# Kernel tuning notes

Measured on AMD Instinct MI355X. Metric: run time of the kernel, lower is better.

## Reference

```python
import jax, jax.numpy as jnp
import numpy as np

BLOCK_SIZE = 50  # from module globals


def setup_inputs() -> dict:
    key = jax.random.key(0)
    ks = jax.random.split(key, 5)
    B, T, C, H = 8, 1024, 512, 64
    return {
        "x": jax.random.normal(ks[0], (B, T, C), dtype=jnp.float32),
        "Wq": jax.random.normal(ks[1], (C, H), dtype=jnp.float32) * (C ** -0.5),
        "Wk": jax.random.normal(ks[2], (C, H), dtype=jnp.float32) * (C ** -0.5),
        "Wv": jax.random.normal(ks[3], (C, H), dtype=jnp.float32) * (C ** -0.5),
        "rel_pos_emb": jax.random.normal(ks[4], (2 * BLOCK_SIZE - 1, H), dtype=jnp.float32),
    }


def reference(x, Wq, Wk, Wv, rel_pos_emb):
    # x: [B, T, C]; dropout is identity in eval mode.
    B, T, C = x.shape
    q = x @ Wq  # [B, T, H]
    k = x @ Wk
    v = x @ Wv
    H = q.shape[-1]

    # relative position indices, clamped to window, shifted to [0, 2*block-2]
    t = jnp.arange(T)
    rel = jnp.clip(t[None, :] - t[:, None], -(BLOCK_SIZE - 1), BLOCK_SIZE - 1) + (BLOCK_SIZE - 1)
    E = rel_pos_emb[rel]  # [T, T, H]

    scale = H ** -0.5
    # content scores (scaled) + relative-position bias (unscaled, per source)
    wei = jnp.einsum("btd,bsd->bts", q, k) * scale + jnp.einsum("btd,tsd->bts", q, E)

    causal = t[None, :] <= t[:, None]  # [T, T] lower-triangular True
    wei = jnp.where(causal[None, :, :], wei, -jnp.inf)
    wei = jax.nn.softmax(wei, axis=-1)
    return jnp.einsum("bts,bsd->btd", wei, v)
```

## Files before the change

kernel.cpp:

```cpp
#include <hip/hip_runtime.h>
#include <hip/hip_bf16.h>

typedef __bf16 bf16x8 __attribute__((ext_vector_type(8)));
typedef float  f32x4  __attribute__((ext_vector_type(4)));

#define MFMA16(a, b, c) __builtin_amdgcn_mfma_f32_16x16x32_bf16(a, b, c, 0, 0, 0)

static __device__ __forceinline__ f32x4 zero4() {
    f32x4 z = {0.f, 0.f, 0.f, 0.f}; return z;
}

#define FIXED_MAX 37.0f

__global__ __launch_bounds__(512) void prep_kernel(
        const float* __restrict__ x,
        const float* __restrict__ Wq, const float* __restrict__ Wk,
        const float* __restrict__ Wv, const float* __restrict__ rpe,
        __bf16* __restrict__ WT_hi, __bf16* __restrict__ WT_lo,
        __bf16* __restrict__ xh, __bf16* __restrict__ xl) {
    int blk = blockIdx.x, tid = threadIdx.x;
    if (blk < 256) {
        int n = blk, k = tid;
        float v;
        if (n < 192) {
            const float* src; int nc;
            if (n < 64)       { src = Wq; nc = n; }
            else if (n < 128) { src = Wk; nc = n - 64; }
            else              { src = Wv; nc = n - 128; }
            v = src[k * 64 + nc];
        } else {
            int nc = n - 192;
            const f32x4* rp = (const f32x4*)(rpe + nc * 64);
            const f32x4* w0 = (const f32x4*)(Wq + k * 64);
            float a0 = 0.f;
#pragma unroll
            for (int i = 0; i < 16; i++) {
                f32x4 r = rp[i], x0 = w0[i];
                a0 += x0.x * r.x + x0.y * r.y + x0.z * r.z + x0.w * r.w;
            }
            v = a0;
        }
        __bf16 h = (__bf16)v;
        WT_hi[n * 512 + k] = h;
        WT_lo[n * 512 + k] = (__bf16)(v - (float)h);
    } else {
        size_t base = (size_t)(blk - 256) * 4096;
        const f32x4* xp = (const f32x4*)(x + base);
        f32x4 a0 = xp[2 * tid], a1 = xp[2 * tid + 1];
        bf16x8 h8, l8;
#pragma unroll
        for (int e = 0; e < 4; e++) {
            float v = a0[e]; __bf16 h = (__bf16)v;
            h8[e] = h; l8[e] = (__bf16)(v - (float)h);
            v = a1[e]; h = (__bf16)v;
            h8[4 + e] = h; l8[4 + e] = (__bf16)(v - (float)h);
        }
        *(bf16x8*)(xh + base + (size_t)tid * 8) = h8;
        *(bf16x8*)(xl + base + (size_t)tid * 8) = l8;
    }
}

__global__ __launch_bounds__(512) void proj_kernel(
        const __bf16* __restrict__ xh, const __bf16* __restrict__ xl,
        const __bf16* __restrict__ WT_hi, const __bf16* __restrict__ WT_lo,
        __bf16* __restrict__ qb, __bf16* __restrict__ kb,
        __bf16* __restrict__ vtb, float* __restrict__ qEg) {
    __shared__ f32x4 accx[4][64][4];

    int tid = threadIdx.x;
    int lane = tid & 63, w = tid >> 6;
    int c = w & 3, kh = w >> 2;
    int l15 = lane & 15, kg = lane >> 4;
    int rowA = blockIdx.x * 16 + l15;
    const __bf16* xhrow = xh + (size_t)rowA * 512;
    const __bf16* xlrow = xl + (size_t)rowA * 512;

    f32x4 acc[4];
#pragma unroll
    for (int i = 0; i < 4; i++) acc[i] = zero4();

#pragma unroll
    for (int ks8 = 0; ks8 < 8; ks8++) {
        int k0 = (kh * 8 + ks8) * 32 + kg * 8;
        bf16x8 xhf = *(const bf16x8*)(xhrow + k0);
        bf16x8 xlf = *(const bf16x8*)(xlrow + k0);
#pragma unroll
        for (int i = 0; i < 4; i++) {
            int nt = c + 4 * i;
            const __bf16* bp = WT_hi + (size_t)(nt * 16 + l15) * 512 + k0;
            bf16x8 bh = *(const bf16x8*)bp;
            acc[i] = MFMA16(xhf, bh, acc[i]);
            if (i == 0 || i == 3) {
                bf16x8 bl = *(const bf16x8*)(WT_lo + (size_t)(nt * 16 + l15) * 512 + k0);
                acc[i] = MFMA16(xhf, bl, acc[i]);
                acc[i] = MFMA16(xlf, bh, acc[i]);
            }
        }
    }

    if (kh == 1) {
#pragma unroll
        for (int i = 0; i < 4; i++) accx[c][lane][i] = acc[i];
    }
    __syncthreads();
    if (kh == 0) {
#pragma unroll
        for (int i = 0; i < 4; i++) {
            f32x4 o = accx[c][lane][i];
            acc[i].x += o.x; acc[i].y += o.y; acc[i].z += o.z; acc[i].w += o.w;
        }
        int rowO = blockIdx.x * 16 + kg * 4;
#pragma unroll
        for (int i = 0; i < 4; i++) {
            int cc = (c * 16 + l15) & 63;
#pragma unroll
            for (int r = 0; r < 4; r++) {
                float v = acc[i][r];
                int row = rowO + r;
                if (i == 0) {
                    qb[row * 64 + cc] = (__bf16)v;
                } else if (i == 1) {
                    kb[row * 64 + cc] = (__bf16)v;
                } else if (i == 2) {
                    int bb = row >> 10, s = row & 1023;
                    vtb[((size_t)(bb * 64 + cc) << 10) + s] = (__bf16)v;
                } else {
                    qEg[row * 64 + cc] = v;
                }
            }
        }
    }
}

__global__ __launch_bounds__(512) void attn_kernel(
        const __bf16* __restrict__ qb, const __bf16* __restrict__ kb,
        const __bf16* __restrict__ vtb, const float* __restrict__ qEg,
        float* __restrict__ out) {
    __shared__ float  Opart[8][16][68];
    __shared__ float  lpart[8][16];
    __shared__ float  qEs[16][52];
    __shared__ __bf16 Plds[8][16][72];

    int tid = threadIdx.x;
    int lane = tid & 63, w = tid >> 6;
    int l15 = lane & 15, kg = lane >> 4;
    int b = blockIdx.x & 7, p = blockIdx.x >> 3;
    int bT = b << 10;
    const __bf16* vbase = vtb + ((size_t)b << 16);

    int qts0 = 63 - p, qts1 = p;
#pragma unroll 1
    for (int qi = 0; qi < 2; qi++) {
        int qt = (qi == 0) ? qts0 : qts1;

        for (int idx = tid; idx < 16 * 50; idx += 512) {
            int r = idx / 50, j = idx - r * 50;
            qEs[r][j] = qEg[(bT + qt * 16 + r) * 64 + j];
        }
        __syncthreads();

        int qrow = bT + qt * 16 + l15;
        bf16x8 qf0 = *(const bf16x8*)(qb + (size_t)qrow * 64 + kg * 8);
        bf16x8 qf1 = *(const bf16x8*)(qb + (size_t)qrow * 64 + 32 + kg * 8);

        f32x4 O[4]; float prs[4];
#pragma unroll
        for (int i = 0; i < 4; i++) { O[i] = zero4(); prs[i] = 0.f; }

        int nt = (qt >> 2) + 1;
        for (int it = w; it < nt; it += 8) {
            int sb = it * 64;
            f32x4 s[4];
#pragma unroll
            for (int ct = 0; ct < 4; ct++) {
                const __bf16* kp = kb + (size_t)(bT + sb + ct * 16 + l15) * 64 + kg * 8;
                bf16x8 kf0 = *(const bf16x8*)kp;
                bf16x8 kf1 = *(const bf16x8*)(kp + 32);
                f32x4 z = zero4();
                z = MFMA16(qf0, kf0, z);
                s[ct] = MFMA16(qf1, kf1, z);
            }

            float pm[4][4];
#pragma unroll
            for (int r = 0; r < 4; r++) {
                int tg = qt * 16 + kg * 4 + r;
#pragma unroll
                for (int ct = 0; ct < 4; ct++) {
                    int sg = sb + ct * 16 + l15;
                    int d = sg - tg;
                    int j = d < -49 ? -49 : d;
                    j = (j > 0 ? 0 : j) + 49;
                    float lg = s[ct][r] * 0.125f + qEs[kg * 4 + r][j] - FIXED_MAX;
                    float pv = (d > 0) ? 0.f : __expf(lg);
                    pm[r][ct] = pv;
                    prs[r] += pv;
                }
            }

#pragma unroll
            for (int r = 0; r < 4; r++)
#pragma unroll
                for (int ct = 0; ct < 4; ct++)
                    Plds[w][kg * 4 + r][ct * 16 + l15] = (__bf16)pm[r][ct];

#pragma unroll
            for (int ks = 0; ks < 2; ks++) {
                bf16x8 af = *(const bf16x8*)&Plds[w][l15][ks * 32 + kg * 8];
#pragma unroll
                for (int dt = 0; dt < 4; dt++) {
                    bf16x8 vf = *(const bf16x8*)(vbase +
                        ((size_t)(dt * 16 + l15) << 10) + sb + ks * 32 + kg * 8);
                    O[dt] = MFMA16(af, vf, O[dt]);
                }
            }
        }

#pragma unroll
        for (int r = 0; r < 4; r++) {
            float v = prs[r];
            v += __shfl_xor(v, 1);
            v += __shfl_xor(v, 2);
            v += __shfl_xor(v, 4);
            v += __shfl_xor(v, 8);
            if (l15 == 0) lpart[w][kg * 4 + r] = v;
#pragma unroll
            for (int dt = 0; dt < 4; dt++)
                Opart[w][kg * 4 + r][dt * 16 + l15] = O[dt][r];
        }
        __syncthreads();

#pragma unroll
        for (int e = 0; e < 2; e++) {
            int elem = tid + e * 512;
            int row = elem >> 6, d = elem & 63;
            float os = 0.f, ls = 0.f;
#pragma unroll
            for (int wv = 0; wv < 8; wv++) {
                os += Opart[wv][row][d];
                ls += lpart[wv][row];
            }
            out[(size_t)(bT + qt * 16 + row) * 64 + d] = os / ls;
        }
        __syncthreads();
    }
}

extern "C" void kernel_launch(void* const* d_in, const int* in_sizes, int n_in,
                              void* d_out, int out_size, void* d_ws, size_t ws_size,
                              hipStream_t stream) {
    const float* x   = (const float*)d_in[0];
    const float* Wq  = (const float*)d_in[1];
    const float* Wk  = (const float*)d_in[2];
    const float* Wv  = (const float*)d_in[3];
    const float* rpe = (const float*)d_in[4];

    char* ws = (char*)d_ws;
    __bf16* WT_hi = (__bf16*)(ws);
    __bf16* WT_lo = (__bf16*)(ws + (256 << 10));
    __bf16* qbuf  = (__bf16*)(ws + (512 << 10));
    __bf16* kbuf  = (__bf16*)(ws + (1536 << 10));
    __bf16* vtb   = (__bf16*)(ws + (2560 << 10));
    float*  qEg   = (float*)(ws + (3584 << 10));
    __bf16* xhb   = (__bf16*)(ws + (6 << 20));
    __bf16* xlb   = (__bf16*)(ws + (14 << 20));
    float*  outp  = (float*)d_out;

    hipLaunchKernelGGL(prep_kernel, dim3(1280), dim3(512), 0, stream,
                       x, Wq, Wk, Wv, rpe, WT_hi, WT_lo, xhb, xlb);
    hipLaunchKernelGGL(proj_kernel, dim3(512), dim3(512), 0, stream,
                       xhb, xlb, WT_hi, WT_lo, qbuf, kbuf, vtb, qEg);
    hipLaunchKernelGGL(attn_kernel, dim3(256), dim3(512), 0, stream,
                       qbuf, kbuf, vtb, qEg, outp);
}
```

Baseline: 122.9 us.

## Fuse prep, projection and attention into one cooperative kernel with grid syncs

Replaces the three launches with one cooperative kernel of 256 blocks that uses grid.sync between phases. The x hi/lo bf16 split now goes into swizzled shared memory instead of a global scratch buffer, and each block projects 32 rows without the split-K LDS reduction. This removes launch gaps and the global round trip of the split x buffers. In exchange it adds grid-wide barrier cost, fewer blocks and waves in the projection phase, and 64KB of LDS per block that may limit occupancy.

```diff
diff --git a/kernel.cpp b/kernel.cpp
--- a/kernel.cpp
+++ b/kernel.cpp
@@ -1,5 +1,8 @@
 #include <hip/hip_runtime.h>
 #include <hip/hip_bf16.h>
+#include <hip/hip_cooperative_groups.h>
+
+namespace cg = cooperative_groups;
 
 typedef __bf16 bf16x8 __attribute__((ext_vector_type(8)));
 typedef float  f32x4  __attribute__((ext_vector_type(4)));
@@ -12,14 +15,32 @@
 
 #define FIXED_MAX 37.0f
 
-__global__ __launch_bounds__(512) void prep_kernel(
+union SMem {
+    struct { char xh[32768]; char xl[32768]; } p12;
+    struct {
+        float  Opart[8][16][68];
+        float  lpart[8][16];
+        float  qEs[16][52];
+        __bf16 Plds[8][16][72];
+    } p3;
+};
+
+__global__ __launch_bounds__(512) void fused_kernel(
         const float* __restrict__ x,
         const float* __restrict__ Wq, const float* __restrict__ Wk,
         const float* __restrict__ Wv, const float* __restrict__ rpe,
         __bf16* __restrict__ WT_hi, __bf16* __restrict__ WT_lo,
-        __bf16* __restrict__ xh, __bf16* __restrict__ xl) {
+        __bf16* __restrict__ qb, __bf16* __restrict__ kb,
+        __bf16* __restrict__ vtb, float* __restrict__ qEg,
+        float* __restrict__ out) {
+    __shared__ SMem sm;
+    cg::grid_group grid = cg::this_grid();
+
     int blk = blockIdx.x, tid = threadIdx.x;
-    if (blk < 256) {
+    int lane = tid & 63, w = tid >> 6;
+    int l15 = lane & 15, kg = lane >> 4;
+
+    {
         int n = blk, k = tid;
         float v;
         if (n < 192) {
@@ -43,76 +64,65 @@
         __bf16 h = (__bf16)v;
         WT_hi[n * 512 + k] = h;
         WT_lo[n * 512 + k] = (__bf16)(v - (float)h);
-    } else {
-        size_t base = (size_t)(blk - 256) * 4096;
-        const f32x4* xp = (const f32x4*)(x + base);
-        f32x4 a0 = xp[2 * tid], a1 = xp[2 * tid + 1];
-        bf16x8 h8, l8;
-#pragma unroll
-        for (int e = 0; e < 4; e++) {
-            float v = a0[e]; __bf16 h = (__bf16)v;
-            h8[e] = h; l8[e] = (__bf16)(v - (float)h);
-            v = a1[e]; h = (__bf16)v;
-            h8[4 + e] = h; l8[4 + e] = (__bf16)(v - (float)h);
-        }
-        *(bf16x8*)(xh + base + (size_t)tid * 8) = h8;
-        *(bf16x8*)(xl + base + (size_t)tid * 8) = l8;
-    }
-}
-
-__global__ __launch_bounds__(512) void proj_kernel(
-        const __bf16* __restrict__ xh, const __bf16* __restrict__ xl,
-        const __bf16* __restrict__ WT_hi, const __bf16* __restrict__ WT_lo,
-        __bf16* __restrict__ qb, __bf16* __restrict__ kb,
-        __bf16* __restrict__ vtb, float* __restrict__ qEg) {
-    __shared__ f32x4 accx[4][64][4];
-
-    int tid = threadIdx.x;
-    int lane = tid & 63, w = tid >> 6;
-    int c = w & 3, kh = w >> 2;
-    int l15 = lane & 15, kg = lane >> 4;
-    int rowA = blockIdx.x * 16 + l15;
-    const __bf16* xhrow = xh + (size_t)rowA * 512;
-    const __bf16* xlrow = xl + (size_t)rowA * 512;
-
-    f32x4 acc[4];
-#pragma unroll
-    for (int i = 0; i < 4; i++) acc[i] = zero4();
-
-#pragma unroll
-    for (int ks8 = 0; ks8 < 8; ks8++) {
-        int k0 = (kh * 8 + ks8) * 32 + kg * 8;
-        bf16x8 xhf = *(const bf16x8*)(xhrow + k0);
-        bf16x8 xlf = *(const bf16x8*)(xlrow + k0);
+    }
+
+    {
+        const f32x4* xp = (const f32x4*)(x + (size_t)blk * 16384);
+#pragma unroll
+        for (int j = 0; j < 4; j++) {
+            int c = tid + 512 * j;
+            f32x4 a0 = xp[2 * c], a1 = xp[2 * c + 1];
+            int row = c >> 6;
+            int swz = ((c & 63) * 16) ^ ((row & 7) << 4);
+            bf16x8 h8, l8;
+#pragma unroll
+            for (int e = 0; e < 4; e++) {
+                float v = a0[e]; __bf16 h = (__bf16)v;
+                h8[e] = h; l8[e] = (__bf16)(v - (float)h);
+                v = a1[e]; h = (__bf16)v;
+                h8[4 + e] = h; l8[4 + e] = (__bf16)(v - (float)h);
+            }
+            *(bf16x8*)(sm.p12.xh + row * 1024 + swz) = h8;
+            *(bf16x8*)(sm.p12.xl + row * 1024 + swz) = l8;
+        }
+    }
+    grid.sync();
+
+    {
+        int rg = w >> 2, c = w & 3;
+        int rr = rg * 16 + l15;
+        const char* xhb = sm.p12.xh + rr * 1024;
+        const char* xlb = sm.p12.xl + rr * 1024;
+        int rsw = (rr & 7) << 4;
+
+        f32x4 acc[4];
+#pragma unroll
+        for (int i = 0; i < 4; i++) acc[i] = zero4();
+
+#pragma unroll
+        for (int ks = 0; ks < 16; ks++) {
+            int k0 = ks * 32 + kg * 8;
+            int swz = (k0 * 2) ^ rsw;
+            bf16x8 xhf = *(const bf16x8*)(xhb + swz);
+            bf16x8 xlf = *(const bf16x8*)(xlb + swz);
+#pragma unroll
+            for (int i = 0; i < 4; i++) {
+                int nt = c + 4 * i;
+                const __bf16* bp = WT_hi + (size_t)(nt * 16 + l15) * 512 + k0;
+                bf16x8 bh = *(const bf16x8*)bp;
+                acc[i] = MFMA16(xhf, bh, acc[i]);
+                if (i == 0 || i == 3) {
+                    bf16x8 bl = *(const bf16x8*)(WT_lo +
+                                 (size_t)(nt * 16 + l15) * 512 + k0);
+                    acc[i] = MFMA16(xhf, bl, acc[i]);
+                    acc[i] = MFMA16(xlf, bh, acc[i]);
+                }
+            }
+        }
+        int rowO = blk * 32 + rg * 16 + kg * 4;
+        int cc = c * 16 + l15;
 #pragma unroll
         for (int i = 0; i < 4; i++) {
-            int nt = c + 4 * i;
-            const __bf16* bp = WT_hi + (size_t)(nt * 16 + l15) * 512 + k0;
-            bf16x8 bh = *(const bf16x8*)bp;
-            acc[i] = MFMA16(xhf, bh, acc[i]);
-            if (i == 0 || i == 3) {
-                bf16x8 bl = *(const bf16x8*)(WT_lo + (size_t)(nt * 16 + l15) * 512 + k0);
-                acc[i] = MFMA16(xhf, bl, acc[i]);
-                acc[i] = MFMA16(xlf, bh, acc[i]);
-            }
-        }
-    }
-
-    if (kh == 1) {
-#pragma unroll
-        for (int i = 0; i < 4; i++) accx[c][lane][i] = acc[i];
-    }
-    __syncthreads();
-    if (kh == 0) {
-#pragma unroll
-        for (int i = 0; i < 4; i++) {
-            f32x4 o = accx[c][lane][i];
-            acc[i].x += o.x; acc[i].y += o.y; acc[i].z += o.z; acc[i].w += o.w;
-        }
-        int rowO = blockIdx.x * 16 + kg * 4;
-#pragma unroll
-        for (int i = 0; i < 4; i++) {
-            int cc = (c * 16 + l15) & 63;
 #pragma unroll
             for (int r = 0; r < 4; r++) {
                 float v = acc[i][r];
@@ -130,119 +140,114 @@
             }
         }
     }
-}
-
-__global__ __launch_bounds__(512) void attn_kernel(
-        const __bf16* __restrict__ qb, const __bf16* __restrict__ kb,
-        const __bf16* __restrict__ vtb, const float* __restrict__ qEg,
-        float* __restrict__ out) {
-    __shared__ float  Opart[8][16][68];
-    __shared__ float  lpart[8][16];
-    __shared__ float  qEs[16][52];
-    __shared__ __bf16 Plds[8][16][72];
-
-    int tid = threadIdx.x;
-    int lane = tid & 63, w = tid >> 6;
-    int l15 = lane & 15, kg = lane >> 4;
-    int b = blockIdx.x & 7, p = blockIdx.x >> 3;
-    int bT = b << 10;
-    const __bf16* vbase = vtb + ((size_t)b << 16);
-
-    int qts0 = 63 - p, qts1 = p;
+    grid.sync();
+
+    {
+        int b = blk & 7, p = blk >> 3;
+        int bT = b << 10;
+        const __bf16* vbase = vtb + ((size_t)b << 16);
+
+        int qts0 = 63 - p, qts1 = p;
 #pragma unroll 1
-    for (int qi = 0; qi < 2; qi++) {
-        int qt = (qi == 0) ? qts0 : qts1;
-
-        for (int idx = tid; idx < 16 * 50; idx += 512) {
-            int r = idx / 50, j = idx - r * 50;
-            qEs[r][j] = qEg[(bT + qt * 16 + r) * 64 + j];
-        }
-        __syncthreads();
-
-        int qrow = bT + qt * 16 + l15;
-        bf16x8 qf0 = *(const bf16x8*)(qb + (size_t)qrow * 64 + kg * 8);
-        bf16x8 qf1 = *(const bf16x8*)(qb + (size_t)qrow * 64 + 32 + kg * 8);
-
-        f32x4 O[4]; float prs[4];
-#pragma unroll
-        for (int i = 0; i < 4; i++) { O[i] = zero4(); prs[i] = 0.f; }
-
-        int nt = (qt >> 2) + 1;
-        for (int it = w; it < nt; it += 8) {
-            int sb = it * 64;
-            f32x4 s[4];
-#pragma unroll
-            for (int ct = 0; ct < 4; ct++) {
-                const __bf16* kp = kb + (size_t)(bT + sb + ct * 16 + l15) * 64 + kg * 8;
-                bf16x8 kf0 = *(const bf16x8*)kp;
-                bf16x8 kf1 = *(const bf16x8*)(kp + 32);
-                f32x4 z = zero4();
-                z = MFMA16(qf0, kf0, z);
-                s[ct] = MFMA16(qf1, kf1, z);
-            }
-
-            float pm[4][4];
+        for (int qi = 0; qi < 2; qi++) {
+            int qt = (qi == 0) ? qts0 : qts1;
+
+            for (int idx = tid; idx < 16 * 50; idx += 512) {
+                int r = idx / 50, j = idx - r * 50;
+                sm.p3.qEs[r][j] = qEg[(bT + qt * 16 + r) * 64 + j];
+            }
+            __syncthreads();
+
+            int qrow = bT + qt * 16 + l15;
+            bf16x8 qf0 = *(const bf16x8*)(qb + (size_t)qrow * 64 + kg * 8);
+            bf16x8 qf1 = *(const bf16x8*)(qb + (size_t)qrow * 64 + 32 + kg * 8);
+
+            f32x4 O[4]; float prs[4];
+#pragma unroll
+            for (int i = 0; i < 4; i++) { O[i] = zero4(); prs[i] = 0.f; }
+
+            int nt = (qt >> 2) + 1;
+            for (int it = w; it < nt; it += 8) {
+                int sb = it * 64;
+                f32x4 s[4];
+#pragma unroll
+                for (int ct = 0; ct < 4; ct++) {
+                    const __bf16* kp = kb +
+                        (size_t)(bT + sb + ct * 16 + l15) * 64 + kg * 8;
+                    bf16x8 kf0 = *(const bf16x8*)kp;
+                    bf16x8 kf1 = *(const bf16x8*)(kp + 32);
+                    f32x4 z = zero4();
+                    z = MFMA16(qf0, kf0, z);
+                    s[ct] = MFMA16(qf1, kf1, z);
+                }
+
+                float pm[4][4];
+#pragma unroll
+                for (int r = 0; r < 4; r++) {
+                    int tg = qt * 16 + kg * 4 + r;
+#pragma unroll
+                    for (int ct = 0; ct < 4; ct++) {
+                        int sg = sb + ct * 16 + l15;
+                        int d = sg - tg;
+                        int j = d < -49 ? -49 : d;
+                        j = (j > 0 ? 0 : j) + 49;
+                        float lg = s[ct][r] * 0.125f +
+                                   sm.p3.qEs[kg * 4 + r][j] - FIXED_MAX;
+                        float pv = (d > 0) ? 0.f : __expf(lg);
+                        pm[r][ct] = pv;
+                        prs[r] += pv;
+                    }
+                }
+
+#pragma unroll
+                for (int r = 0; r < 4; r++)
+#pragma unroll
+                    for (int ct = 0; ct < 4; ct++)
+                        sm.p3.Plds[w][kg * 4 + r][ct * 16 + l15] =
+                            (__bf16)pm[r][ct];
+
+#pragma unroll
+                for (int ks = 0; ks < 2; ks++) {
+                    bf16x8 af = *(const bf16x8*)
+                        &sm.p3.Plds[w][l15][ks * 32 + kg * 8];
+#pragma unroll
+                    for (int dt = 0; dt < 4; dt++) {
+                        bf16x8 vf = *(const bf16x8*)(vbase +
+                            ((size_t)(dt * 16 + l15) << 10) + sb +
+                            ks * 32 + kg * 8);
+                        O[dt] = MFMA16(af, vf, O[dt]);
+                    }
+                }
+            }
+
 #pragma unroll
             for (int r = 0; r < 4; r++) {
-                int tg = qt * 16 + kg * 4 + r;
-#pragma unroll
-                for (int ct = 0; ct < 4; ct++) {
-                    int sg = sb + ct * 16 + l15;
-                    int d = sg - tg;
-                    int j = d < -49 ? -49 : d;
-                    j = (j > 0 ? 0 : j) + 49;
-                    float lg = s[ct][r] * 0.125f + qEs[kg * 4 + r][j] - FIXED_MAX;
-                    float pv = (d > 0) ? 0.f : __expf(lg);
-                    pm[r][ct] = pv;
-                    prs[r] += pv;
-                }
-            }
-
-#pragma unroll
-            for (int r = 0; r < 4; r++)
-#pragma unroll
-                for (int ct = 0; ct < 4; ct++)
-                    Plds[w][kg * 4 + r][ct * 16 + l15] = (__bf16)pm[r][ct];
-
-#pragma unroll
-            for (int ks = 0; ks < 2; ks++) {
-                bf16x8 af = *(const bf16x8*)&Plds[w][l15][ks * 32 + kg * 8];
-#pragma unroll
-                for (int dt = 0; dt < 4; dt++) {
-                    bf16x8 vf = *(const bf16x8*)(vbase +
-                        ((size_t)(dt * 16 + l15) << 10) + sb + ks * 32 + kg * 8);
-                    O[dt] = MFMA16(af, vf, O[dt]);
-                }
-            }
-        }
-
-#pragma unroll
-        for (int r = 0; r < 4; r++) {
-            float v = prs[r];
-            v += __shfl_xor(v, 1);
-            v += __shfl_xor(v, 2);
-            v += __shfl_xor(v, 4);
-            v += __shfl_xor(v, 8);
-            if (l15 == 0) lpart[w][kg * 4 + r] = v;
-#pragma unroll
-            for (int dt = 0; dt < 4; dt++)
-                Opart[w][kg * 4 + r][dt * 16 + l15] = O[dt][r];
-        }
-        __syncthreads();
-
-#pragma unroll
-        for (int e = 0; e < 2; e++) {
-            int elem = tid + e * 512;
-            int row = elem >> 6, d = elem & 63;
-            float os = 0.f, ls = 0.f;
-#pragma unroll
-            for (int wv = 0; wv < 8; wv++) {
-                os += Opart[wv][row][d];
-                ls += lpart[wv][row];
-            }
-            out[(size_t)(bT + qt * 16 + row) * 64 + d] = os / ls;
-        }
-        __syncthreads();
+                float v = prs[r];
+                v += __shfl_xor(v, 1);
+                v += __shfl_xor(v, 2);
+                v += __shfl_xor(v, 4);
+                v += __shfl_xor(v, 8);
+                if (l15 == 0) sm.p3.lpart[w][kg * 4 + r] = v;
+#pragma unroll
+                for (int dt = 0; dt < 4; dt++)
+                    sm.p3.Opart[w][kg * 4 + r][dt * 16 + l15] = O[dt][r];
+            }
+            __syncthreads();
+
+#pragma unroll
+            for (int e = 0; e < 2; e++) {
+                int elem = tid + e * 512;
+                int row = elem >> 6, d = elem & 63;
+                float os = 0.f, ls = 0.f;
+#pragma unroll
+                for (int wv = 0; wv < 8; wv++) {
+                    os += sm.p3.Opart[wv][row][d];
+                    ls += sm.p3.lpart[wv][row];
+                }
+                out[(size_t)(bT + qt * 16 + row) * 64 + d] = os / ls;
+            }
+            __syncthreads();
+        }
     }
 }
 
@@ -262,14 +267,12 @@
     __bf16* kbuf  = (__bf16*)(ws + (1536 << 10));
     __bf16* vtb   = (__bf16*)(ws + (2560 << 10));
     float*  qEg   = (float*)(ws + (3584 << 10));
-    __bf16* xhb   = (__bf16*)(ws + (6 << 20));
-    __bf16* xlb   = (__bf16*)(ws + (14 << 20));
     float*  outp  = (float*)d_out;
 
-    hipLaunchKernelGGL(prep_kernel, dim3(1280), dim3(512), 0, stream,
-                       x, Wq, Wk, Wv, rpe, WT_hi, WT_lo, xhb, xlb);
-    hipLaunchKernelGGL(proj_kernel, dim3(512), dim3(512), 0, stream,
-                       xhb, xlb, WT_hi, WT_lo, qbuf, kbuf, vtb, qEg);
-    hipLaunchKernelGGL(attn_kernel, dim3(256), dim3(512), 0, stream,
-                       qbuf, kbuf, vtb, qEg, outp);
+    void* args[] = { (void*)&x, (void*)&Wq, (void*)&Wk, (void*)&Wv,
+                     (void*)&rpe, (void*)&WT_hi, (void*)&WT_lo,
+                     (void*)&qbuf, (void*)&kbuf, (void*)&vtb,
+                     (void*)&qEg, (void*)&outp };
+    hipLaunchCooperativeKernel((const void*)fused_kernel,
+                               dim3(256), dim3(512), args, 0, stream);
 }
```

Measured after the change: 187.1 us. 52.2% more time.
